# Optimization experiments

Hardware: AMD Instinct MI355X
Metric: run time of the kernel (lower is better)

The kernel has to match this reference:

```python
import jax, jax.numpy as jnp
import numpy as np

IN_F, OUT_F, H = 128, 256, 4
D = OUT_F // H  # head_dim = 64
NEG_SLOPE = 0.2


def setup_inputs() -> dict:
    key = jax.random.key(0)
    k1, k2, k3, k4 = jax.random.split(key, 4)
    B, N = 8, 1024
    node_features = jax.random.normal(k1, (B, N, IN_F), dtype=jnp.float32)
    adjacency_matrix = jax.random.randint(k2, (B, N, N), 0, 2, dtype=jnp.int32)
    # W: torch Linear(in,out,bias=False) weight is [out,in]; store as [in,out] for x @ W
    W = jax.random.normal(k3, (IN_F, OUT_F), dtype=jnp.float32) * (1.0 / np.sqrt(IN_F))
    # attention: Linear(2*head_dim, 1, bias=False) -> vector of length 2*D, shared across heads
    a = jax.random.normal(k4, (2 * D,), dtype=jnp.float32) * (1.0 / np.sqrt(2 * D))
    return {"node_features": node_features, "adjacency_matrix": adjacency_matrix, "W": W, "a": a}


def reference(node_features, adjacency_matrix, W, a):
    B, N, _ = node_features.shape
    h = (node_features @ W).reshape(B, N, H, D)  # [B,N,H,D]
    # attention(concat(h_i, h_j)) == <h_i, a[:D]> + <h_j, a[D:]> (same math, no [B,N,N,H,2D] concat)
    s_i = jnp.einsum('bnhd,d->bnh', h, a[:D])  # score contrib of target node i
    s_j = jnp.einsum('bnhd,d->bnh', h, a[D:])  # score contrib of source node j
    e = s_i[:, :, None, :] + s_j[:, None, :, :]  # [B,N,N,H]
    e = jnp.where(e >= 0, e, NEG_SLOPE * e)  # LeakyReLU(0.2)
    mask = adjacency_matrix[..., None] != 0  # [B,N,N,1] -> broadcast over heads
    e = jnp.where(mask, e, -jnp.inf)
    alpha = jax.nn.softmax(e, axis=2)  # softmax over source nodes j
    out = jnp.einsum('bijh,bjhd->bihd', alpha, h)  # weighted sum over j
    return out.reshape(B, N, OUT_F)  # concat=True
```

## Files before the change

### kernel.cpp

```cpp
#include <hip/hip_runtime.h>
#include <hip/hip_bf16.h>
#include <math.h>

constexpr int IN_F = 128, OUT_F = 256, NH = 4, HD = 64;
constexpr int B = 8, N = 1024;
#define NEG 0.2f

typedef __attribute__((ext_vector_type(8))) short bf16x8;
typedef __attribute__((ext_vector_type(4))) float f32x4;
typedef __attribute__((ext_vector_type(8))) unsigned short u16x8;

static __device__ __forceinline__ short f2bf(float f) {
    __hip_bfloat16 b = __float2bfloat16(f);
    return *reinterpret_cast<short*>(&b);
}

__global__ __launch_bounds__(256) void k_pack(
    const int* __restrict__ adj,
    unsigned* __restrict__ pkdT)
{
    __shared__ unsigned tr[32][33];
    const int bid = blockIdx.x;
    const int b = bid >> 5, ch = bid & 31;
    const int t = threadIdx.x, lane = t & 63, w = t >> 6;
    const int n0 = ch * 32;

    for (int rr = 0; rr < 8; ++rr) {
        const int rloc = w * 8 + rr;
        const int* __restrict__ src = adj + ((size_t)b * N + n0 + rloc) * N;
        unsigned myw = 0;
#pragma unroll
        for (int c = 0; c < 16; ++c) {
            const unsigned long long m = __ballot(src[c * 64 + lane] != 0);
            const unsigned lo = (unsigned)m, hi = (unsigned)(m >> 32);
            if ((lane >> 1) == c) myw = (lane & 1) ? hi : lo;
        }
        if (lane < 32) tr[rloc][lane] = myw;
    }
    __syncthreads();

    const int w2 = t >> 3, r4 = (t & 7) * 4;
    uint4 v;
    v.x = tr[r4 + 0][w2]; v.y = tr[r4 + 1][w2];
    v.z = tr[r4 + 2][w2]; v.w = tr[r4 + 3][w2];
    unsigned* __restrict__ dst = pkdT + ((size_t)(b * 16 + (ch >> 1))) * 32 * 64
                               + (size_t)w2 * 64 + (ch & 1) * 32 + r4;
    *(uint4*)dst = v;
}

__global__ __launch_bounds__(256) void k_gemm(
    const float* __restrict__ x,
    const float* __restrict__ W,
    const float* __restrict__ a,
    unsigned short* __restrict__ hT,
    float* __restrict__ siT,
    float* __restrict__ sjT)
{
    constexpr int ROWS = 8;
    __shared__ float xs[ROWS][IN_F];
    const int t = threadIdx.x;
    const int row0 = blockIdx.x * ROWS;

    ((float4*)xs)[t] = ((const float4*)(x + (size_t)row0 * IN_F))[t];
    __syncthreads();

    float acc[ROWS];
#pragma unroll
    for (int r = 0; r < ROWS; ++r) acc[r] = 0.f;
    for (int k = 0; k < IN_F; ++k) {
        const float w = W[k * OUT_F + t];
#pragma unroll
        for (int r = 0; r < ROWS; ++r) acc[r] = fmaf(xs[r][k], w, acc[r]);
    }

    const int lane = t & 63, head = t >> 6, d = t & 63;
    const int b = row0 >> 10, n0 = row0 & (N - 1);

    u16x8 pk;
#pragma unroll
    for (int r = 0; r < ROWS; ++r) pk[r] = (unsigned short)f2bf(acc[r]);
    *(u16x8*)&hT[((size_t)(b * NH + head) * HD + d) * N + n0] = pk;

    const float ai = a[lane], aj = a[HD + lane];
#pragma unroll
    for (int r = 0; r < ROWS; ++r) {
        float si = acc[r] * ai;
        float sj = acc[r] * aj;
#pragma unroll
        for (int off = 32; off; off >>= 1) {
            si += __shfl_xor(si, off, 64);
            sj += __shfl_xor(sj, off, 64);
        }
        if (lane == 0) {
            siT[(size_t)(b * NH + head) * N + n0 + r] = si;
            sjT[(size_t)(b * NH + head) * N + n0 + r] = sj;
        }
    }
}

__global__ __launch_bounds__(256, 3) void k_pv(
    const unsigned short* __restrict__ hT,
    const float* __restrict__ siT,
    const float* __restrict__ sjT,
    const unsigned* __restrict__ pkdT,
    float* __restrict__ out)
{
    constexpr int TJ = 64, NIT = N / TJ, PADJ = 72;
    __shared__ __align__(16) short ht[2][64 * PADJ];
    __shared__ float sjs[N];
    __shared__ unsigned pwl[32 * 64];
    __shared__ float zbuf[4][16];

    const int bid = blockIdx.x;
    const int it = bid & 15, h = (bid >> 4) & 3, b = bid >> 6;
    const int t = threadIdx.x, lane = t & 63, w = t >> 6;
    const int i0 = it * 64;

    ((float4*)sjs)[t] = ((const float4*)(sjT + (size_t)(b * NH + h) * N))[t];
    {
        const uint4* ps = (const uint4*)(pkdT + ((size_t)(b * 16 + it)) * 32 * 64);
        ((uint4*)pwl)[t] = ps[t];
        ((uint4*)pwl)[t + 256] = ps[t + 256];
    }

    const int il = lane & 15, q = lane >> 4, qc = q * 8;
    const int lr = w * 16 + il;
    const float si = siT[(size_t)(b * NH + h) * N + i0 + lr];

    const int srow = t >> 2, sc = (t & 3) * 16;
    const unsigned short* __restrict__ hsrc =
        hT + (size_t)(b * NH + h) * HD * N + (size_t)srow * N + sc;
    short* const hd0 = &ht[0][srow * PADJ + sc];
    short* const hd1 = &ht[1][srow * PADJ + sc];

    f32x4 acc0 = {0.f,0.f,0.f,0.f}, acc1 = {0.f,0.f,0.f,0.f};
    f32x4 acc2 = {0.f,0.f,0.f,0.f}, acc3 = {0.f,0.f,0.f,0.f};
    float psA = 0.f, psB = 0.f;

    u16x8 ra = *(const u16x8*)(hsrc);
    u16x8 rc = *(const u16x8*)(hsrc + 8);

    for (int itr = 0; itr < NIT; ++itr) {
        short* const hd = (itr & 1) ? hd1 : hd0;
        *(u16x8*)hd = ra;
        *(u16x8*)(hd + 8) = rc;

        const int jn = ((itr + 1) & (NIT - 1)) * TJ;
        ra = *(const u16x8*)(hsrc + jn);
        rc = *(const u16x8*)(hsrc + jn + 8);

        __syncthreads();
        const short* const hb = (itr & 1) ? ht[1] : ht[0];
        const int j0 = itr * TJ;

#define STEP(ks, PS)                                                         \
        {                                                                    \
            const unsigned byte = (pwl[(2 * itr + (ks)) * 64 + lr] >> qc) & 0xffu; \
            const int jq = j0 + (ks) * 32 + qc;                              \
            const float4 s0 = *(const float4*)&sjs[jq];                      \
            const float4 s1 = *(const float4*)&sjs[jq + 4];                  \
            const float sv[8] = {s0.x,s0.y,s0.z,s0.w,s1.x,s1.y,s1.z,s1.w};   \
            bf16x8 af;                                                       \
            _Pragma("unroll")                                                \
            for (int e = 0; e < 8; ++e) {                                    \
                const float ev0 = si + sv[e];                                \
                const float ev = fmaxf(ev0, NEG * ev0);                      \
                const float pe = ((byte >> e) & 1u) ? __expf(ev) : 0.f;      \
                PS += pe;                                                    \
                af[e] = f2bf(pe);                                            \
            }                                                                \
            const bf16x8 b0 = *(const bf16x8*)&hb[(0*16 + il)*PADJ + (ks)*32 + qc]; \
            const bf16x8 b1 = *(const bf16x8*)&hb[(1*16 + il)*PADJ + (ks)*32 + qc]; \
            const bf16x8 b2 = *(const bf16x8*)&hb[(2*16 + il)*PADJ + (ks)*32 + qc]; \
            const bf16x8 b3 = *(const bf16x8*)&hb[(3*16 + il)*PADJ + (ks)*32 + qc]; \
            acc0 = __builtin_amdgcn_mfma_f32_16x16x32_bf16(af, b0, acc0, 0, 0, 0); \
            acc1 = __builtin_amdgcn_mfma_f32_16x16x32_bf16(af, b1, acc1, 0, 0, 0); \
            acc2 = __builtin_amdgcn_mfma_f32_16x16x32_bf16(af, b2, acc2, 0, 0, 0); \
            acc3 = __builtin_amdgcn_mfma_f32_16x16x32_bf16(af, b3, acc3, 0, 0, 0); \
        }
        STEP(0, psA)
        STEP(1, psB)
#undef STEP
        __syncthreads();
    }

    float ps = psA + psB;
    ps += __shfl_xor(ps, 16, 64);
    ps += __shfl_xor(ps, 32, 64);
    if (lane < 16) zbuf[w][lane] = ps;
    __syncthreads();

    float iz[4];
#pragma unroll
    for (int r = 0; r < 4; ++r) iz[r] = 1.f / zbuf[w][q * 4 + r];

    float* __restrict__ ob = out + ((size_t)b * N + i0 + w * 16) * OUT_F + h * HD + il;
#pragma unroll
    for (int r = 0; r < 4; ++r) {
        float* o = ob + (size_t)(q * 4 + r) * OUT_F;
        o[0]  = acc0[r] * iz[r];
        o[16] = acc1[r] * iz[r];
        o[32] = acc2[r] * iz[r];
        o[48] = acc3[r] * iz[r];
    }
}

extern "C" void kernel_launch(void* const* d_in, const int* in_sizes, int n_in,
                              void* d_out, int out_size, void* d_ws, size_t ws_size,
                              hipStream_t stream) {
    const float* x   = (const float*)d_in[0];
    const int*   adj = (const int*)d_in[1];
    const float* W   = (const float*)d_in[2];
    const float* a   = (const float*)d_in[3];
    float* out = (float*)d_out;

    unsigned short* hT = (unsigned short*)d_ws;
    float* siT = (float*)(hT + (size_t)B * NH * HD * N);
    float* sjT = siT + (size_t)B * NH * N;
    unsigned* pkdT = (unsigned*)(sjT + (size_t)B * NH * N);

    k_pack<<<B * 32, 256, 0, stream>>>(adj, pkdT);
    k_gemm<<<B * N / 8, 256, 0, stream>>>(x, W, a, hT, siT, sjT);
    k_pv<<<B * NH * (N / 64), 256, 0, stream>>>(hT, siT, sjT, pkdT, out);
}
```

Before: 47.93 us.

## Split attention source dimension across two blocks with atomic accumulation and normalize pass

The PV kernel now splits the source-node loop into two halves, doubling the grid, and each block atomically adds its partial outputs and softmax denominators into global buffers. A new normalization kernel divides by the accumulated denominators afterwards, and output and Z are zeroed with memsets. Block indexing in all kernels is also reordered to interleave batches, and the occupancy hint is raised. This adds atomics, two memsets and an extra kernel launch in exchange for more parallelism. It keeps the existing unshifted exponent with no running max.

```diff
diff --git a/kernel.cpp b/kernel.cpp
--- a/kernel.cpp
+++ b/kernel.cpp
@@ -21,7 +21,7 @@
 {
     __shared__ unsigned tr[32][33];
     const int bid = blockIdx.x;
-    const int b = bid >> 5, ch = bid & 31;
+    const int b = bid & 7, ch = bid >> 3;
     const int t = threadIdx.x, lane = t & 63, w = t >> 6;
     const int n0 = ch * 32;
 
@@ -59,7 +59,9 @@
     constexpr int ROWS = 8;
     __shared__ float xs[ROWS][IN_F];
     const int t = threadIdx.x;
-    const int row0 = blockIdx.x * ROWS;
+    const int bid = blockIdx.x;
+    const int b = bid & 7, rg = bid >> 3;
+    const int row0 = b * N + rg * ROWS;
 
     ((float4*)xs)[t] = ((const float4*)(x + (size_t)row0 * IN_F))[t];
     __syncthreads();
@@ -74,7 +76,7 @@
     }
 
     const int lane = t & 63, head = t >> 6, d = t & 63;
-    const int b = row0 >> 10, n0 = row0 & (N - 1);
+    const int n0 = rg * ROWS;
 
     u16x8 pk;
 #pragma unroll
@@ -98,29 +100,31 @@
     }
 }
 
-__global__ __launch_bounds__(256, 3) void k_pv(
+__global__ __launch_bounds__(256, 4) void k_pv(
     const unsigned short* __restrict__ hT,
     const float* __restrict__ siT,
     const float* __restrict__ sjT,
     const unsigned* __restrict__ pkdT,
-    float* __restrict__ out)
-{
-    constexpr int TJ = 64, NIT = N / TJ, PADJ = 72;
+    float* __restrict__ out,
+    float* __restrict__ Z)
+{
+    constexpr int TJ = 64, NIT = 8, PADJ = 72;
     __shared__ __align__(16) short ht[2][64 * PADJ];
     __shared__ float sjs[N];
-    __shared__ unsigned pwl[32 * 64];
-    __shared__ float zbuf[4][16];
+    __shared__ unsigned pwl[16 * 64];
 
     const int bid = blockIdx.x;
-    const int it = bid & 15, h = (bid >> 4) & 3, b = bid >> 6;
+    const int b = bid & 7, r = bid >> 3;
+    const int h = r & 3, itile = (r >> 2) & 15, jh = (r >> 6) & 1;
     const int t = threadIdx.x, lane = t & 63, w = t >> 6;
-    const int i0 = it * 64;
+    const int i0 = itile * 64;
+    const int jbase = jh << 9;
 
     ((float4*)sjs)[t] = ((const float4*)(sjT + (size_t)(b * NH + h) * N))[t];
     {
-        const uint4* ps = (const uint4*)(pkdT + ((size_t)(b * 16 + it)) * 32 * 64);
+        const uint4* ps = (const uint4*)(pkdT + ((size_t)(b * 16 + itile)) * 32 * 64
+                                         + (size_t)jh * 16 * 64);
         ((uint4*)pwl)[t] = ps[t];
-        ((uint4*)pwl)[t + 256] = ps[t + 256];
     }
 
     const int il = lane & 15, q = lane >> 4, qc = q * 8;
@@ -129,7 +133,7 @@
 
     const int srow = t >> 2, sc = (t & 3) * 16;
     const unsigned short* __restrict__ hsrc =
-        hT + (size_t)(b * NH + h) * HD * N + (size_t)srow * N + sc;
+        hT + (size_t)(b * NH + h) * HD * N + (size_t)srow * N + sc + jbase;
     short* const hd0 = &ht[0][srow * PADJ + sc];
     short* const hd1 = &ht[1][srow * PADJ + sc];
 
@@ -151,7 +155,7 @@
 
         __syncthreads();
         const short* const hb = (itr & 1) ? ht[1] : ht[0];
-        const int j0 = itr * TJ;
+        const int j0 = jbase + itr * TJ;
 
 #define STEP(ks, PS)                                                         \
         {                                                                    \
@@ -187,22 +191,34 @@
     float ps = psA + psB;
     ps += __shfl_xor(ps, 16, 64);
     ps += __shfl_xor(ps, 32, 64);
-    if (lane < 16) zbuf[w][lane] = ps;
-    __syncthreads();
-
-    float iz[4];
-#pragma unroll
-    for (int r = 0; r < 4; ++r) iz[r] = 1.f / zbuf[w][q * 4 + r];
+    if (lane < 16)
+        atomicAdd(&Z[(size_t)(b * NH + h) * N + i0 + w * 16 + lane], ps);
 
     float* __restrict__ ob = out + ((size_t)b * N + i0 + w * 16) * OUT_F + h * HD + il;
 #pragma unroll
-    for (int r = 0; r < 4; ++r) {
-        float* o = ob + (size_t)(q * 4 + r) * OUT_F;
-        o[0]  = acc0[r] * iz[r];
-        o[16] = acc1[r] * iz[r];
-        o[32] = acc2[r] * iz[r];
-        o[48] = acc3[r] * iz[r];
-    }
+    for (int rr = 0; rr < 4; ++rr) {
+        float* o = ob + (size_t)(q * 4 + rr) * OUT_F;
+        atomicAdd(&o[0],  acc0[rr]);
+        atomicAdd(&o[16], acc1[rr]);
+        atomicAdd(&o[32], acc2[rr]);
+        atomicAdd(&o[48], acc3[rr]);
+    }
+}
+
+__global__ __launch_bounds__(256) void k_norm(
+    float* __restrict__ out,
+    const float* __restrict__ Z)
+{
+    const int idx = blockIdx.x * 256 + threadIdx.x;
+    const int fi = idx * 4;
+    const int ng = fi >> 8;
+    const int c = fi & 255, h = c >> 6;
+    const int b = ng >> 10, n = ng & (N - 1);
+    const float z = Z[((size_t)(b * NH + h)) * N + n];
+    const float s = 1.f / z;
+    float4 v = ((float4*)out)[idx];
+    v.x *= s; v.y *= s; v.z *= s; v.w *= s;
+    ((float4*)out)[idx] = v;
 }
 
 extern "C" void kernel_launch(void* const* d_in, const int* in_sizes, int n_in,
@@ -218,8 +234,13 @@
     float* siT = (float*)(hT + (size_t)B * NH * HD * N);
     float* sjT = siT + (size_t)B * NH * N;
     unsigned* pkdT = (unsigned*)(sjT + (size_t)B * NH * N);
+    float* Z = (float*)(pkdT + (size_t)B * 16 * 32 * 64);
+
+    hipMemsetAsync(out, 0, (size_t)out_size * sizeof(float), stream);
+    hipMemsetAsync(Z, 0, (size_t)B * NH * N * sizeof(float), stream);
 
     k_pack<<<B * 32, 256, 0, stream>>>(adj, pkdT);
     k_gemm<<<B * N / 8, 256, 0, stream>>>(x, W, a, hT, siT, sjT);
-    k_pv<<<B * NH * (N / 64), 256, 0, stream>>>(hT, siT, sjT, pkdT, out);
-}
+    k_pv<<<B * NH * (N / 64) * 2, 256, 0, stream>>>(hT, siT, sjT, pkdT, out, Z);
+    k_norm<<<(B * N * OUT_F / 4) / 256, 256, 0, stream>>>(out, Z);
+}
```

Result: slower. 61.70 us (+28.7%).

## Split head dim across blocks, keep adjacency bits in registers, drop per-iteration sync

Applied to the files above, without the earlier changes.

The attention-value kernel now splits the 64-wide head dimension into two 32-wide halves across separate blocks, doubling the grid. The packed adjacency words move from shared memory into 32 per-thread registers, and the trailing barrier in the double-buffered loop is removed. Occupancy rises to 4 blocks per SM. The pack kernel uses a finer 8-row grid, and all kernels interleave the batch index in the low block bits. This raises parallelism and cuts shared memory and barrier cost, at the price of computing the softmax exponentials twice per head and adding register pressure.

```diff
diff --git a/kernel.cpp b/kernel.cpp
--- a/kernel.cpp
+++ b/kernel.cpp
@@ -19,14 +19,15 @@
     const int* __restrict__ adj,
     unsigned* __restrict__ pkdT)
 {
-    __shared__ unsigned tr[32][33];
+    __shared__ unsigned tr[8][33];
     const int bid = blockIdx.x;
-    const int b = bid >> 5, ch = bid & 31;
+    const int b = bid & 7, ch = bid >> 3;
     const int t = threadIdx.x, lane = t & 63, w = t >> 6;
-    const int n0 = ch * 32;
-
-    for (int rr = 0; rr < 8; ++rr) {
-        const int rloc = w * 8 + rr;
+    const int n0 = ch * 8;
+
+#pragma unroll
+    for (int rr = 0; rr < 2; ++rr) {
+        const int rloc = w * 2 + rr;
         const int* __restrict__ src = adj + ((size_t)b * N + n0 + rloc) * N;
         unsigned myw = 0;
 #pragma unroll
@@ -39,13 +40,10 @@
     }
     __syncthreads();
 
-    const int w2 = t >> 3, r4 = (t & 7) * 4;
-    uint4 v;
-    v.x = tr[r4 + 0][w2]; v.y = tr[r4 + 1][w2];
-    v.z = tr[r4 + 2][w2]; v.w = tr[r4 + 3][w2];
-    unsigned* __restrict__ dst = pkdT + ((size_t)(b * 16 + (ch >> 1))) * 32 * 64
-                               + (size_t)w2 * 64 + (ch & 1) * 32 + r4;
-    *(uint4*)dst = v;
+    const int w2 = t >> 3, r = t & 7;
+    unsigned* __restrict__ dst = pkdT + ((size_t)(b * 16 + (n0 >> 6))) * 32 * 64
+                               + (size_t)w2 * 64 + (n0 & 63) + r;
+    *dst = tr[r][w2];
 }
 
 __global__ __launch_bounds__(256) void k_gemm(
@@ -59,7 +57,9 @@
     constexpr int ROWS = 8;
     __shared__ float xs[ROWS][IN_F];
     const int t = threadIdx.x;
-    const int row0 = blockIdx.x * ROWS;
+    const int bid = blockIdx.x;
+    const int b = bid & 7, rg = bid >> 3;
+    const int row0 = b * N + rg * ROWS;
 
     ((float4*)xs)[t] = ((const float4*)(x + (size_t)row0 * IN_F))[t];
     __syncthreads();
@@ -74,7 +74,7 @@
     }
 
     const int lane = t & 63, head = t >> 6, d = t & 63;
-    const int b = row0 >> 10, n0 = row0 & (N - 1);
+    const int n0 = rg * ROWS;
 
     u16x8 pk;
 #pragma unroll
@@ -98,7 +98,7 @@
     }
 }
 
-__global__ __launch_bounds__(256, 3) void k_pv(
+__global__ __launch_bounds__(256, 4) void k_pv(
     const unsigned short* __restrict__ hT,
     const float* __restrict__ siT,
     const float* __restrict__ sjT,
@@ -106,57 +106,54 @@
     float* __restrict__ out)
 {
     constexpr int TJ = 64, NIT = N / TJ, PADJ = 72;
-    __shared__ __align__(16) short ht[2][64 * PADJ];
+    __shared__ __align__(16) short ht[2][32 * PADJ];
     __shared__ float sjs[N];
-    __shared__ unsigned pwl[32 * 64];
     __shared__ float zbuf[4][16];
 
     const int bid = blockIdx.x;
-    const int it = bid & 15, h = (bid >> 4) & 3, b = bid >> 6;
+    const int b = bid & 7, r = bid >> 3;
+    const int h = r & 3, itile = (r >> 2) & 15, dh = (r >> 6) & 1;
     const int t = threadIdx.x, lane = t & 63, w = t >> 6;
-    const int i0 = it * 64;
+    const int i0 = itile * 64;
 
     ((float4*)sjs)[t] = ((const float4*)(sjT + (size_t)(b * NH + h) * N))[t];
-    {
-        const uint4* ps = (const uint4*)(pkdT + ((size_t)(b * 16 + it)) * 32 * 64);
-        ((uint4*)pwl)[t] = ps[t];
-        ((uint4*)pwl)[t + 256] = ps[t + 256];
-    }
 
     const int il = lane & 15, q = lane >> 4, qc = q * 8;
     const int lr = w * 16 + il;
     const float si = siT[(size_t)(b * NH + h) * N + i0 + lr];
 
-    const int srow = t >> 2, sc = (t & 3) * 16;
+    unsigned bw[32];
+    {
+        const unsigned* __restrict__ pb = pkdT + ((size_t)(b * 16 + itile)) * 32 * 64 + lr;
+#pragma unroll
+        for (int k = 0; k < 32; ++k) bw[k] = pb[(size_t)k * 64];
+    }
+
+    const int srow = t >> 3, sc = (t & 7) * 8;
     const unsigned short* __restrict__ hsrc =
-        hT + (size_t)(b * NH + h) * HD * N + (size_t)srow * N + sc;
+        hT + (size_t)(b * NH + h) * HD * N + (size_t)(dh * 32 + srow) * N + sc;
     short* const hd0 = &ht[0][srow * PADJ + sc];
     short* const hd1 = &ht[1][srow * PADJ + sc];
 
     f32x4 acc0 = {0.f,0.f,0.f,0.f}, acc1 = {0.f,0.f,0.f,0.f};
-    f32x4 acc2 = {0.f,0.f,0.f,0.f}, acc3 = {0.f,0.f,0.f,0.f};
     float psA = 0.f, psB = 0.f;
 
     u16x8 ra = *(const u16x8*)(hsrc);
-    u16x8 rc = *(const u16x8*)(hsrc + 8);
-
+
+#pragma unroll
     for (int itr = 0; itr < NIT; ++itr) {
         short* const hd = (itr & 1) ? hd1 : hd0;
         *(u16x8*)hd = ra;
-        *(u16x8*)(hd + 8) = rc;
-
         const int jn = ((itr + 1) & (NIT - 1)) * TJ;
         ra = *(const u16x8*)(hsrc + jn);
-        rc = *(const u16x8*)(hsrc + jn + 8);
 
         __syncthreads();
         const short* const hb = (itr & 1) ? ht[1] : ht[0];
-        const int j0 = itr * TJ;
 
 #define STEP(ks, PS)                                                         \
         {                                                                    \
-            const unsigned byte = (pwl[(2 * itr + (ks)) * 64 + lr] >> qc) & 0xffu; \
-            const int jq = j0 + (ks) * 32 + qc;                              \
+            const unsigned byte = (bw[2 * itr + (ks)] >> qc) & 0xffu;        \
+            const int jq = itr * TJ + (ks) * 32 + qc;                        \
             const float4 s0 = *(const float4*)&sjs[jq];                      \
             const float4 s1 = *(const float4*)&sjs[jq + 4];                  \
             const float sv[8] = {s0.x,s0.y,s0.z,s0.w,s1.x,s1.y,s1.z,s1.w};   \
@@ -169,39 +166,34 @@
                 PS += pe;                                                    \
                 af[e] = f2bf(pe);                                            \
             }                                                                \
-            const bf16x8 b0 = *(const bf16x8*)&hb[(0*16 + il)*PADJ + (ks)*32 + qc]; \
-            const bf16x8 b1 = *(const bf16x8*)&hb[(1*16 + il)*PADJ + (ks)*32 + qc]; \
-            const bf16x8 b2 = *(const bf16x8*)&hb[(2*16 + il)*PADJ + (ks)*32 + qc]; \
-            const bf16x8 b3 = *(const bf16x8*)&hb[(3*16 + il)*PADJ + (ks)*32 + qc]; \
+            const bf16x8 b0 = *(const bf16x8*)&hb[(il) * PADJ + (ks)*32 + qc];      \
+            const bf16x8 b1 = *(const bf16x8*)&hb[(16 + il) * PADJ + (ks)*32 + qc]; \
             acc0 = __builtin_amdgcn_mfma_f32_16x16x32_bf16(af, b0, acc0, 0, 0, 0); \
             acc1 = __builtin_amdgcn_mfma_f32_16x16x32_bf16(af, b1, acc1, 0, 0, 0); \
-            acc2 = __builtin_amdgcn_mfma_f32_16x16x32_bf16(af, b2, acc2, 0, 0, 0); \
-            acc3 = __builtin_amdgcn_mfma_f32_16x16x32_bf16(af, b3, acc3, 0, 0, 0); \
         }
         STEP(0, psA)
         STEP(1, psB)
 #undef STEP
-        __syncthreads();
     }
 
     float ps = psA + psB;
     ps += __shfl_xor(ps, 16, 64);
     ps += __shfl_xor(ps, 32, 64);
+    __syncthreads();
     if (lane < 16) zbuf[w][lane] = ps;
     __syncthreads();
 
     float iz[4];
 #pragma unroll
-    for (int r = 0; r < 4; ++r) iz[r] = 1.f / zbuf[w][q * 4 + r];
-
-    float* __restrict__ ob = out + ((size_t)b * N + i0 + w * 16) * OUT_F + h * HD + il;
-#pragma unroll
-    for (int r = 0; r < 4; ++r) {
-        float* o = ob + (size_t)(q * 4 + r) * OUT_F;
-        o[0]  = acc0[r] * iz[r];
-        o[16] = acc1[r] * iz[r];
-        o[32] = acc2[r] * iz[r];
-        o[48] = acc3[r] * iz[r];
+    for (int rr = 0; rr < 4; ++rr) iz[rr] = 1.f / zbuf[w][q * 4 + rr];
+
+    float* __restrict__ ob = out + ((size_t)b * N + i0 + w * 16) * OUT_F
+                           + h * HD + dh * 32 + il;
+#pragma unroll
+    for (int rr = 0; rr < 4; ++rr) {
+        float* o = ob + (size_t)(q * 4 + rr) * OUT_F;
+        o[0]  = acc0[rr] * iz[rr];
+        o[16] = acc1[rr] * iz[rr];
     }
 }
 
@@ -219,7 +211,7 @@
     float* sjT = siT + (size_t)B * NH * N;
     unsigned* pkdT = (unsigned*)(sjT + (size_t)B * NH * N);
 
-    k_pack<<<B * 32, 256, 0, stream>>>(adj, pkdT);
+    k_pack<<<B * 128, 256, 0, stream>>>(adj, pkdT);
     k_gemm<<<B * N / 8, 256, 0, stream>>>(x, W, a, hT, siT, sjT);
-    k_pv<<<B * NH * (N / 64), 256, 0, stream>>>(hT, siT, sjT, pkdT, out);
-}
+    k_pv<<<B * NH * 16 * 2, 256, 0, stream>>>(hT, siT, sjT, pkdT, out);
+}
```

New measurement: 52.20 us. 8.9% more time.
